# Optimization experiments

Hardware: AMD Instinct MI355X
Metric: run time of the kernel (lower is better)

## Reference

```python
import jax, jax.numpy as jnp
import numpy as np

N = 2_000_000
FEAT = 83      # mat_feature_len
DIMF = 64      # dim_features
LAT = 32       # latent_dim
INIT_RANGE = 0.02
SHIFT_INIT = 0.001
EPS = 1e-12


def setup_inputs() -> dict:
    key = jax.random.key(0)
    ks = jax.random.split(key, 8)
    inputs = jax.random.normal(ks[0], (N, FEAT), dtype=jnp.float32)
    keep = jax.random.bernoulli(ks[1], 0.5, (N,))
    inputs = inputs * keep[:, None].astype(jnp.float32)
    shift = jnp.full((1,), SHIFT_INIT, dtype=jnp.float32)  # ZeroShift scalar
    W1 = jax.random.normal(ks[2], (FEAT, DIMF), dtype=jnp.float32) * INIT_RANGE
    b1 = jnp.zeros((DIMF,), dtype=jnp.float32)
    Wh0 = jax.random.normal(ks[3], (DIMF, LAT), dtype=jnp.float32) * INIT_RANGE
    bh0 = jnp.zeros((LAT,), dtype=jnp.float32)
    Wh1 = jax.random.normal(ks[4], (LAT, LAT), dtype=jnp.float32) * INIT_RANGE
    bh1 = jnp.zeros((LAT,), dtype=jnp.float32)
    return {"inputs": inputs, "shift": shift, "W1": W1, "b1": b1,
            "Wh0": Wh0, "bh0": bh0, "Wh1": Wh1, "bh1": bh1}


def reference(inputs, shift, W1, b1, Wh0, bh0, Wh1, bh1):
    # mask_zero: a material row is valid iff any feature is nonzero
    mask = jnp.any(inputs != 0, axis=-1)  # (N,)
    # Original gathers valid rows, runs MLP, scatters back (zeros elsewhere).
    # All ops are row-wise, so compute densely and zero masked rows — same math.
    x = inputs + shift                            # ZeroShift (scalar shift)
    x = jax.nn.relu(x @ W1 + b1)                  # dens_1 -> (N, DIMF)
    x = jax.nn.relu(x @ Wh0 + bh0)                # hidden 0 -> (N, LAT)
    x = jax.nn.relu(x @ Wh1 + bh1)                # hidden 1 -> (N, LAT)
    # UnifyVector: L2-normalize rows
    norm = jnp.sqrt(jnp.sum(x * x, axis=-1, keepdims=True))
    emb = x / jnp.maximum(norm, EPS)
    emb = emb * mask[:, None].astype(emb.dtype)   # scatter_nd equivalent
    return (emb, emb, emb)
```

## Files before the change

kernel.cpp:

```cpp
#include <hip/hip_runtime.h>

#define FEAT 83
#define DIMF 64
#define LAT  32
#define THREADS 256
#define RPB  128

typedef __attribute__((ext_vector_type(8))) short bf16x8;
typedef __attribute__((ext_vector_type(4))) float f32x4;
typedef __attribute__((ext_vector_type(4))) unsigned u32x4;

#define WT1H 0
#define WT1L 6144
#define WT2H 12288
#define WT2L 14336
#define WT3H 16384
#define WT3L 17408
#define WS_SHORTS 18432

#define SM_SHORTS 26880

__device__ __forceinline__ short f2b(float f) {
    unsigned u = __float_as_uint(f);
    u += 0x7fffu + ((u >> 16) & 1u);
    return (short)(u >> 16);
}
__device__ __forceinline__ float b2f(short h) {
    return __uint_as_float(((unsigned)(unsigned short)h) << 16);
}

__global__ void prep_weights(const float* __restrict__ W1,
                             const float* __restrict__ Wh0,
                             const float* __restrict__ Wh1,
                             short* __restrict__ ws)
{
    const int stride = gridDim.x * blockDim.x;
    const int tid = blockIdx.x * blockDim.x + threadIdx.x;
    for (int idx = tid; idx < 64 * 96; idx += stride) {
        int c = idx / 96, k = idx - c * 96;
        float w = (k < FEAT) ? W1[k * 64 + c] : 0.f;
        short hi = f2b(w);
        ws[WT1H + idx] = hi;
        ws[WT1L + idx] = f2b(w - b2f(hi));
    }
    for (int idx = tid; idx < 32 * 64; idx += stride) {
        int c = idx >> 6, k = idx & 63;
        float w = Wh0[k * 32 + c];
        short hi = f2b(w);
        ws[WT2H + idx] = hi;
        ws[WT2L + idx] = f2b(w - b2f(hi));
    }
    for (int idx = tid; idx < 32 * 32; idx += stride) {
        int c = idx >> 5, k = idx & 31;
        float w = Wh1[k * 32 + c];
        short hi = f2b(w);
        ws[WT3H + idx] = hi;
        ws[WT3L + idx] = f2b(w - b2f(hi));
    }
}

__device__ __forceinline__ void unpack8(const unsigned* p, bf16x8& hi, bf16x8& lo) {
    union { bf16x8 v; unsigned u[4]; } H, L;
    #pragma unroll
    for (int d = 0; d < 4; ++d) {
        H.u[d] = __builtin_amdgcn_perm(p[2 * d + 1], p[2 * d], 0x07060302u);
        L.u[d] = __builtin_amdgcn_perm(p[2 * d + 1], p[2 * d], 0x05040100u);
    }
    hi = H.v; lo = L.v;
}

__global__ __launch_bounds__(THREADS, 3)
void material_encoder_kernel(const float* __restrict__ inp,
                             const float* __restrict__ shiftp,
                             const short* __restrict__ ws,
                             const float* __restrict__ b1,
                             const float* __restrict__ bh0,
                             const float* __restrict__ bh1,
                             float* __restrict__ out,
                             int nrows)
{
    __shared__ __align__(16) short sm[SM_SHORTS];
    unsigned* scr = (unsigned*)((char*)sm + 36864) + (threadIdx.x >> 6) * 1024;
    float* maskf  = (float*)((char*)sm + 53248);

    const int t    = threadIdx.x;
    const int lane = t & 63;
    const int wv   = t >> 6;
    const int lr   = lane & 15;
    const int lq   = (lane >> 4) & 3;

    float* xw = (float*)((char*)sm + wv * 10624);

    f32x4 xreg[11];
    {
        const f32x4* __restrict__ src4 = (const f32x4*)
            (inp + (long long)blockIdx.x * (RPB * FEAT) + wv * (32 * FEAT));
        #pragma unroll
        for (int r = 0; r < 10; ++r) xreg[r] = src4[r * 64 + lane];
        if (lane < 24) xreg[10] = src4[640 + lane];
    }
    f32x4 wreg[9];
    {
        const f32x4* __restrict__ wsrc = (const f32x4*)ws;
        #pragma unroll
        for (int it = 0; it < 9; ++it) wreg[it] = wsrc[it * THREADS + t];
    }
    {
        f32x4* xdst = (f32x4*)xw;
        #pragma unroll
        for (int r = 0; r < 10; ++r) xdst[r * 64 + lane] = xreg[r];
        if (lane < 24) xdst[640 + lane] = xreg[10];
    }

    float bias1[4], bias2[2], bias3[2];
    #pragma unroll
    for (int n = 0; n < 4; ++n) bias1[n] = b1[lr + 16 * n];
    #pragma unroll
    for (int n = 0; n < 2; ++n) { bias2[n] = bh0[lr + 16 * n]; bias3[n] = bh1[lr + 16 * n]; }
    const float sh = shiftp[0];
    const int Rw = blockIdx.x * RPB + wv * 32;

    bf16x8 a1h[2][3], a1l[2][3];
    float nzm[2];
    #pragma unroll
    for (int m = 0; m < 2; ++m) {
        const float* __restrict__ xr = xw + (16 * m + lr) * FEAT;
        float nz = 0.f;
        #pragma unroll
        for (int s = 0; s < 3; ++s) {
            const int k0 = 32 * s + 8 * lq;
            bf16x8 fh, fl;
            #pragma unroll
            for (int i = 0; i < 8; ++i) {
                int kk = k0 + i;
                kk = (kk < FEAT) ? kk : (FEAT - 1);
                const float x = xr[kk];
                nz = fmaxf(nz, fabsf(x));
                const float xs = x + sh;
                const unsigned u = __float_as_uint(xs);
                fh[i] = (short)(u >> 16);
                fl[i] = f2b(xs - __uint_as_float(u & 0xffff0000u));
            }
            a1h[m][s] = fh;
            a1l[m][s] = fl;
        }
        nzm[m] = nz;
    }
    #pragma unroll
    for (int m = 0; m < 2; ++m) {
        nzm[m] = fmaxf(nzm[m], __shfl_xor(nzm[m], 16));
        nzm[m] = fmaxf(nzm[m], __shfl_xor(nzm[m], 32));
    }
    if (lq == 0) {
        maskf[wv * 32 + lr]      = nzm[0];
        maskf[wv * 32 + 16 + lr] = nzm[1];
    }

    __syncthreads();

    {
        f32x4* wdst = (f32x4*)sm;
        #pragma unroll
        for (int it = 0; it < 9; ++it) wdst[it * THREADS + t] = wreg[it];
    }
    __syncthreads();

    f32x4 acc[2][4];
    #pragma unroll
    for (int m = 0; m < 2; ++m)
        #pragma unroll
        for (int n = 0; n < 4; ++n)
            acc[m][n] = (f32x4){bias1[n], bias1[n], bias1[n], bias1[n]};

    #pragma unroll
    for (int s = 0; s < 3; ++s)
        #pragma unroll
        for (int n = 0; n < 4; ++n) {
            bf16x8 bh = *(const bf16x8*)&sm[WT1H + (lr + 16 * n) * 96 + 32 * s + 8 * lq];
            bf16x8 bl = *(const bf16x8*)&sm[WT1L + (lr + 16 * n) * 96 + 32 * s + 8 * lq];
            #pragma unroll
            for (int m = 0; m < 2; ++m) {
                acc[m][n] = __builtin_amdgcn_mfma_f32_16x16x32_bf16(a1h[m][s], bh, acc[m][n], 0, 0, 0);
                acc[m][n] = __builtin_amdgcn_mfma_f32_16x16x32_bf16(a1l[m][s], bh, acc[m][n], 0, 0, 0);
                acc[m][n] = __builtin_amdgcn_mfma_f32_16x16x32_bf16(a1h[m][s], bl, acc[m][n], 0, 0, 0);
            }
        }

    f32x4 acc2[2][2];
    #pragma unroll
    for (int m = 0; m < 2; ++m)
        #pragma unroll
        for (int n = 0; n < 2; ++n)
            acc2[m][n] = (f32x4){bias2[n], bias2[n], bias2[n], bias2[n]};

    #pragma unroll
    for (int s = 0; s < 2; ++s) {
        #pragma unroll
        for (int m = 0; m < 2; ++m)
            #pragma unroll
            for (int np = 0; np < 2; ++np)
                #pragma unroll
                for (int r = 0; r < 4; ++r) {
                    const float hv = fmaxf(acc[m][2 * s + np][r], 0.f);
                    const unsigned u = __float_as_uint(hv);
                    const unsigned hiu = u & 0xffff0000u;
                    const unsigned lo16 =
                        (unsigned short)f2b(hv - __uint_as_float(hiu));
                    scr[(16 * m + 4 * lq + r) * 32 + lr + 16 * np] = hiu | lo16;
                }
        bf16x8 a2h[2], a2l[2];
        #pragma unroll
        for (int m = 0; m < 2; ++m) {
            unsigned p[8];
            *(u32x4*)&p[0] = *(const u32x4*)&scr[(lr + 16 * m) * 32 + 8 * lq];
            *(u32x4*)&p[4] = *(const u32x4*)&scr[(lr + 16 * m) * 32 + 8 * lq + 4];
            unpack8(p, a2h[m], a2l[m]);
        }
        #pragma unroll
        for (int n = 0; n < 2; ++n) {
            bf16x8 bh = *(const bf16x8*)&sm[WT2H + (lr + 16 * n) * 64 + 32 * s + 8 * lq];
            bf16x8 bl = *(const bf16x8*)&sm[WT2L + (lr + 16 * n) * 64 + 32 * s + 8 * lq];
            #pragma unroll
            for (int m = 0; m < 2; ++m) {
                acc2[m][n] = __builtin_amdgcn_mfma_f32_16x16x32_bf16(a2h[m], bh, acc2[m][n], 0, 0, 0);
                acc2[m][n] = __builtin_amdgcn_mfma_f32_16x16x32_bf16(a2l[m], bh, acc2[m][n], 0, 0, 0);
                acc2[m][n] = __builtin_amdgcn_mfma_f32_16x16x32_bf16(a2h[m], bl, acc2[m][n], 0, 0, 0);
            }
        }
    }

    f32x4 acc3[2][2];
    #pragma unroll
    for (int m = 0; m < 2; ++m)
        #pragma unroll
        for (int n = 0; n < 2; ++n)
            acc3[m][n] = (f32x4){bias3[n], bias3[n], bias3[n], bias3[n]};

    #pragma unroll
    for (int m = 0; m < 2; ++m)
        #pragma unroll
        for (int n = 0; n < 2; ++n)
            #pragma unroll
            for (int r = 0; r < 4; ++r) {
                const float gv = fmaxf(acc2[m][n][r], 0.f);
                const unsigned u = __float_as_uint(gv);
                const unsigned hiu = u & 0xffff0000u;
                const unsigned lo16 =
                    (unsigned short)f2b(gv - __uint_as_float(hiu));
                scr[(16 * m + 4 * lq + r) * 32 + lr + 16 * n] = hiu | lo16;
            }
    {
        bf16x8 a3h[2], a3l[2];
        #pragma unroll
        for (int m = 0; m < 2; ++m) {
            unsigned p[8];
            *(u32x4*)&p[0] = *(const u32x4*)&scr[(lr + 16 * m) * 32 + 8 * lq];
            *(u32x4*)&p[4] = *(const u32x4*)&scr[(lr + 16 * m) * 32 + 8 * lq + 4];
            unpack8(p, a3h[m], a3l[m]);
        }
        #pragma unroll
        for (int n = 0; n < 2; ++n) {
            bf16x8 bh = *(const bf16x8*)&sm[WT3H + (lr + 16 * n) * 32 + 8 * lq];
            bf16x8 bl = *(const bf16x8*)&sm[WT3L + (lr + 16 * n) * 32 + 8 * lq];
            #pragma unroll
            for (int m = 0; m < 2; ++m) {
                acc3[m][n] = __builtin_amdgcn_mfma_f32_16x16x32_bf16(a3h[m], bh, acc3[m][n], 0, 0, 0);
                acc3[m][n] = __builtin_amdgcn_mfma_f32_16x16x32_bf16(a3l[m], bh, acc3[m][n], 0, 0, 0);
                acc3[m][n] = __builtin_amdgcn_mfma_f32_16x16x32_bf16(a3h[m], bl, acc3[m][n], 0, 0, 0);
            }
        }
    }

    float er[2][2][4];
    float ssq[2][4];
    #pragma unroll
    for (int m = 0; m < 2; ++m)
        #pragma unroll
        for (int r = 0; r < 4; ++r) ssq[m][r] = 0.f;
    #pragma unroll
    for (int m = 0; m < 2; ++m)
        #pragma unroll
        for (int n = 0; n < 2; ++n)
            #pragma unroll
            for (int r = 0; r < 4; ++r) {
                float e = fmaxf(acc3[m][n][r], 0.f);
                er[m][n][r] = e;
                ssq[m][r] = fmaf(e, e, ssq[m][r]);
            }
    #pragma unroll
    for (int msk = 1; msk <= 8; msk <<= 1)
        #pragma unroll
        for (int m = 0; m < 2; ++m)
            #pragma unroll
            for (int r = 0; r < 4; ++r)
                ssq[m][r] += __shfl_xor(ssq[m][r], msk);

    const float* maskp = maskf + wv * 32;
    f32x4 mk[2];
    mk[0] = *(const f32x4*)&maskp[4 * lq];
    mk[1] = *(const f32x4*)&maskp[16 + 4 * lq];

    float sc[2][4];
    #pragma unroll
    for (int m = 0; m < 2; ++m)
        #pragma unroll
        for (int r = 0; r < 4; ++r)
            sc[m][r] = (mk[m][r] != 0.f) ? rsqrtf(fmaxf(ssq[m][r], 1e-24f)) : 0.f;

    const int osz = nrows * LAT;
    float* __restrict__ ob = out + (long long)Rw * LAT;
    #pragma unroll
    for (int m = 0; m < 2; ++m)
        #pragma unroll
        for (int r = 0; r < 4; ++r) {
            const int ro = (16 * m + 4 * lq + r) * LAT;
            #pragma unroll
            for (int n = 0; n < 2; ++n) {
                const float vv = er[m][n][r] * sc[m][r];
                const int cc = ro + lr + 16 * n;
                ob[cc]           = vv;
                ob[osz + cc]     = vv;
                ob[2 * osz + cc] = vv;
            }
        }
}

extern "C" void kernel_launch(void* const* d_in, const int* in_sizes, int n_in,
                              void* d_out, int out_size, void* d_ws, size_t ws_size,
                              hipStream_t stream) {
    const float* inp    = (const float*)d_in[0];
    const float* shiftp = (const float*)d_in[1];
    const float* W1     = (const float*)d_in[2];
    const float* b1     = (const float*)d_in[3];
    const float* Wh0    = (const float*)d_in[4];
    const float* bh0    = (const float*)d_in[5];
    const float* Wh1    = (const float*)d_in[6];
    const float* bh1    = (const float*)d_in[7];
    float* out = (float*)d_out;
    short* ws  = (short*)d_ws;

    const int nrows = in_sizes[0] / FEAT;
    const int blocks = nrows / RPB;

    prep_weights<<<dim3(24), dim3(THREADS), 0, stream>>>(W1, Wh0, Wh1, ws);
    material_encoder_kernel<<<dim3(blocks), dim3(THREADS), 0, stream>>>(
        inp, shiftp, ws, b1, bh0, bh1, out, nrows);
}
```

Before: 265.6 us.

## Read MFMA-fragment-packed weights directly from global memory, drop LDS weight staging

The weight prep kernel now writes the split bf16 weights in the exact per-lane MFMA fragment order, so the main kernel loads B operands straight from global (L2/L1-cached) with coalesced 16-byte loads instead of staging them into shared memory behind two block barriers. The row mask is now passed between lanes with shuffles instead of through LDS, and the block shrinks to 2 waves and 64 rows with about 21KB of LDS. This removes the barriers and the large LDS footprint, which should allow more resident blocks, at the cost of repeated global weight loads per wave that rely on cache hits.

```diff
diff --git a/kernel.cpp b/kernel.cpp
--- a/kernel.cpp
+++ b/kernel.cpp
@@ -3,22 +3,16 @@
 #define FEAT 83
 #define DIMF 64
 #define LAT  32
-#define THREADS 256
-#define RPB  128
+#define THREADS 128
+#define RPB  64
 
 typedef __attribute__((ext_vector_type(8))) short bf16x8;
 typedef __attribute__((ext_vector_type(4))) float f32x4;
 typedef __attribute__((ext_vector_type(4))) unsigned u32x4;
 
-#define WT1H 0
-#define WT1L 6144
-#define WT2H 12288
-#define WT2L 14336
-#define WT3H 16384
-#define WT3L 17408
 #define WS_SHORTS 18432
 
-#define SM_SHORTS 26880
+#define SM_BYTES (2 * 10624)
 
 __device__ __forceinline__ short f2b(float f) {
     unsigned u = __float_as_uint(f);
@@ -36,26 +30,37 @@
 {
     const int stride = gridDim.x * blockDim.x;
     const int tid = blockIdx.x * blockDim.x + threadIdx.x;
-    for (int idx = tid; idx < 64 * 96; idx += stride) {
-        int c = idx / 96, k = idx - c * 96;
-        float w = (k < FEAT) ? W1[k * 64 + c] : 0.f;
+    for (int idx = tid; idx < 12288; idx += stride) {
+        int p = idx >> 10, rem = idx & 1023;
+        int half = rem >> 9, e = rem & 511;
+        int l = e >> 3, i = e & 7;
+        int n = p / 3, s = p - 3 * n;
+        int c = (l & 15) + 16 * n;
+        int k = 32 * s + 8 * ((l >> 4) & 3) + i;
+        float w = (k < FEAT) ? W1[k * DIMF + c] : 0.f;
         short hi = f2b(w);
-        ws[WT1H + idx] = hi;
-        ws[WT1L + idx] = f2b(w - b2f(hi));
-    }
-    for (int idx = tid; idx < 32 * 64; idx += stride) {
-        int c = idx >> 6, k = idx & 63;
-        float w = Wh0[k * 32 + c];
+        ws[idx] = half ? f2b(w - b2f(hi)) : hi;
+    }
+    for (int idx = tid; idx < 4096; idx += stride) {
+        int p = idx >> 10, rem = idx & 1023;
+        int half = rem >> 9, e = rem & 511;
+        int l = e >> 3, i = e & 7;
+        int n = p >> 1, s = p & 1;
+        int c = (l & 15) + 16 * n;
+        int k = 32 * s + 8 * ((l >> 4) & 3) + i;
+        float w = Wh0[k * LAT + c];
         short hi = f2b(w);
-        ws[WT2H + idx] = hi;
-        ws[WT2L + idx] = f2b(w - b2f(hi));
-    }
-    for (int idx = tid; idx < 32 * 32; idx += stride) {
-        int c = idx >> 5, k = idx & 31;
-        float w = Wh1[k * 32 + c];
+        ws[12288 + idx] = half ? f2b(w - b2f(hi)) : hi;
+    }
+    for (int idx = tid; idx < 2048; idx += stride) {
+        int n = idx >> 10, rem = idx & 1023;
+        int half = rem >> 9, e = rem & 511;
+        int l = e >> 3, i = e & 7;
+        int c = (l & 15) + 16 * n;
+        int k = 8 * ((l >> 4) & 3) + i;
+        float w = Wh1[k * LAT + c];
         short hi = f2b(w);
-        ws[WT3H + idx] = hi;
-        ws[WT3L + idx] = f2b(w - b2f(hi));
+        ws[16384 + idx] = half ? f2b(w - b2f(hi)) : hi;
     }
 }
 
@@ -79,9 +84,7 @@
                              float* __restrict__ out,
                              int nrows)
 {
-    __shared__ __align__(16) short sm[SM_SHORTS];
-    unsigned* scr = (unsigned*)((char*)sm + 36864) + (threadIdx.x >> 6) * 1024;
-    float* maskf  = (float*)((char*)sm + 53248);
+    __shared__ __align__(16) char smb[SM_BYTES];
 
     const int t    = threadIdx.x;
     const int lane = t & 63;
@@ -89,7 +92,8 @@
     const int lr   = lane & 15;
     const int lq   = (lane >> 4) & 3;
 
-    float* xw = (float*)((char*)sm + wv * 10624);
+    float*    xw  = (float*)(smb + wv * 10624);
+    unsigned* scr = (unsigned*)(smb + wv * 10624);
 
     f32x4 xreg[11];
     {
@@ -98,12 +102,6 @@
         #pragma unroll
         for (int r = 0; r < 10; ++r) xreg[r] = src4[r * 64 + lane];
         if (lane < 24) xreg[10] = src4[640 + lane];
-    }
-    f32x4 wreg[9];
-    {
-        const f32x4* __restrict__ wsrc = (const f32x4*)ws;
-        #pragma unroll
-        for (int it = 0; it < 9; ++it) wreg[it] = wsrc[it * THREADS + t];
     }
     {
         f32x4* xdst = (f32x4*)xw;
@@ -151,19 +149,8 @@
         nzm[m] = fmaxf(nzm[m], __shfl_xor(nzm[m], 16));
         nzm[m] = fmaxf(nzm[m], __shfl_xor(nzm[m], 32));
     }
-    if (lq == 0) {
-        maskf[wv * 32 + lr]      = nzm[0];
-        maskf[wv * 32 + 16 + lr] = nzm[1];
-    }
-
-    __syncthreads();
-
-    {
-        f32x4* wdst = (f32x4*)sm;
-        #pragma unroll
-        for (int it = 0; it < 9; ++it) wdst[it * THREADS + t] = wreg[it];
-    }
-    __syncthreads();
+
+    const bf16x8* __restrict__ wf = (const bf16x8*)ws;
 
     f32x4 acc[2][4];
     #pragma unroll
@@ -176,8 +163,9 @@
     for (int s = 0; s < 3; ++s)
         #pragma unroll
         for (int n = 0; n < 4; ++n) {
-            bf16x8 bh = *(const bf16x8*)&sm[WT1H + (lr + 16 * n) * 96 + 32 * s + 8 * lq];
-            bf16x8 bl = *(const bf16x8*)&sm[WT1L + (lr + 16 * n) * 96 + 32 * s + 8 * lq];
+            const int p = (n * 3 + s) * 128;
+            bf16x8 bh = wf[p + lane];
+            bf16x8 bl = wf[p + 64 + lane];
             #pragma unroll
             for (int m = 0; m < 2; ++m) {
                 acc[m][n] = __builtin_amdgcn_mfma_f32_16x16x32_bf16(a1h[m][s], bh, acc[m][n], 0, 0, 0);
@@ -218,8 +206,9 @@
         }
         #pragma unroll
         for (int n = 0; n < 2; ++n) {
-            bf16x8 bh = *(const bf16x8*)&sm[WT2H + (lr + 16 * n) * 64 + 32 * s + 8 * lq];
-            bf16x8 bl = *(const bf16x8*)&sm[WT2L + (lr + 16 * n) * 64 + 32 * s + 8 * lq];
+            const int p = 1536 + (n * 2 + s) * 128;
+            bf16x8 bh = wf[p + lane];
+            bf16x8 bl = wf[p + 64 + lane];
             #pragma unroll
             for (int m = 0; m < 2; ++m) {
                 acc2[m][n] = __builtin_amdgcn_mfma_f32_16x16x32_bf16(a2h[m], bh, acc2[m][n], 0, 0, 0);
@@ -260,8 +249,9 @@
         }
         #pragma unroll
         for (int n = 0; n < 2; ++n) {
-            bf16x8 bh = *(const bf16x8*)&sm[WT3H + (lr + 16 * n) * 32 + 8 * lq];
-            bf16x8 bl = *(const bf16x8*)&sm[WT3L + (lr + 16 * n) * 32 + 8 * lq];
+            const int p = 2048 + n * 128;
+            bf16x8 bh = wf[p + lane];
+            bf16x8 bl = wf[p + 64 + lane];
             #pragma unroll
             for (int m = 0; m < 2; ++m) {
                 acc3[m][n] = __builtin_amdgcn_mfma_f32_16x16x32_bf16(a3h[m], bh, acc3[m][n], 0, 0, 0);
@@ -295,17 +285,14 @@
             for (int r = 0; r < 4; ++r)
                 ssq[m][r] += __shfl_xor(ssq[m][r], msk);
 
-    const float* maskp = maskf + wv * 32;
-    f32x4 mk[2];
-    mk[0] = *(const f32x4*)&maskp[4 * lq];
-    mk[1] = *(const f32x4*)&maskp[16 + 4 * lq];
-
     float sc[2][4];
     #pragma unroll
     for (int m = 0; m < 2; ++m)
         #pragma unroll
-        for (int r = 0; r < 4; ++r)
-            sc[m][r] = (mk[m][r] != 0.f) ? rsqrtf(fmaxf(ssq[m][r], 1e-24f)) : 0.f;
+        for (int r = 0; r < 4; ++r) {
+            const float mkv = __shfl(nzm[m], 4 * lq + r);
+            sc[m][r] = (mkv != 0.f) ? rsqrtf(fmaxf(ssq[m][r], 1e-24f)) : 0.f;
+        }
 
     const int osz = nrows * LAT;
     float* __restrict__ ob = out + (long long)Rw * LAT;
@@ -342,7 +329,7 @@
     const int nrows = in_sizes[0] / FEAT;
     const int blocks = nrows / RPB;
 
-    prep_weights<<<dim3(24), dim3(THREADS), 0, stream>>>(W1, Wh0, Wh1, ws);
+    prep_weights<<<dim3(24), dim3(256), 0, stream>>>(W1, Wh0, Wh1, ws);
     material_encoder_kernel<<<dim3(blocks), dim3(THREADS), 0, stream>>>(
         inp, shiftp, ws, b1, bh0, bh1, out, nrows);
 }
```

After: 306.9 us. +15.6%, slower.

## Convert to persistent grid-stride kernel with register prefetch of next tile

Applied to the files above, without the earlier changes.

Replaces one-block-per-128-rows launch with a persistent grid of 512 blocks of 128 threads, each looping over 64-row tiles with the next tile's input prefetched into registers while the MFMA chain runs. Weights are loaded into shared memory once per block instead of once per tile, and the input staging area is double-buffered per wave. The mask is now kept in registers via shuffles instead of shared memory. The risk is lower occupancy (launch bounds 1, 512 small blocks on 256 CUs) which may reduce memory-level parallelism for this bandwidth-bound kernel.

```diff
diff --git a/kernel.cpp b/kernel.cpp
--- a/kernel.cpp
+++ b/kernel.cpp
@@ -3,8 +3,9 @@
 #define FEAT 83
 #define DIMF 64
 #define LAT  32
-#define THREADS 256
-#define RPB  128
+#define THREADS 128
+#define TROWS 64
+#define GRID 512
 
 typedef __attribute__((ext_vector_type(8))) short bf16x8;
 typedef __attribute__((ext_vector_type(4))) float f32x4;
@@ -18,7 +19,7 @@
 #define WT3L 17408
 #define WS_SHORTS 18432
 
-#define SM_SHORTS 26880
+#define SM_BYTES (36864 + 2 * 21248)
 
 __device__ __forceinline__ short f2b(float f) {
     unsigned u = __float_as_uint(f);
@@ -69,7 +70,7 @@
     hi = H.v; lo = L.v;
 }
 
-__global__ __launch_bounds__(THREADS, 3)
+__global__ __launch_bounds__(THREADS, 1)
 void material_encoder_kernel(const float* __restrict__ inp,
                              const float* __restrict__ shiftp,
                              const short* __restrict__ ws,
@@ -79,9 +80,8 @@
                              float* __restrict__ out,
                              int nrows)
 {
-    __shared__ __align__(16) short sm[SM_SHORTS];
-    unsigned* scr = (unsigned*)((char*)sm + 36864) + (threadIdx.x >> 6) * 1024;
-    float* maskf  = (float*)((char*)sm + 53248);
+    __shared__ __align__(16) char smb[SM_BYTES];
+    short* sm = (short*)smb;
 
     const int t    = threadIdx.x;
     const int lane = t & 63;
@@ -89,27 +89,12 @@
     const int lr   = lane & 15;
     const int lq   = (lane >> 4) & 3;
 
-    float* xw = (float*)((char*)sm + wv * 10624);
-
-    f32x4 xreg[11];
-    {
-        const f32x4* __restrict__ src4 = (const f32x4*)
-            (inp + (long long)blockIdx.x * (RPB * FEAT) + wv * (32 * FEAT));
-        #pragma unroll
-        for (int r = 0; r < 10; ++r) xreg[r] = src4[r * 64 + lane];
-        if (lane < 24) xreg[10] = src4[640 + lane];
-    }
-    f32x4 wreg[9];
     {
         const f32x4* __restrict__ wsrc = (const f32x4*)ws;
-        #pragma unroll
-        for (int it = 0; it < 9; ++it) wreg[it] = wsrc[it * THREADS + t];
-    }
-    {
-        f32x4* xdst = (f32x4*)xw;
-        #pragma unroll
-        for (int r = 0; r < 10; ++r) xdst[r * 64 + lane] = xreg[r];
-        if (lane < 24) xdst[640 + lane] = xreg[10];
+        f32x4* wdst = (f32x4*)smb;
+        #pragma unroll
+        for (int it = 0; it < 18; ++it)
+            wdst[it * THREADS + t] = wsrc[it * THREADS + t];
     }
 
     float bias1[4], bias2[2], bias3[2];
@@ -118,211 +103,237 @@
     #pragma unroll
     for (int n = 0; n < 2; ++n) { bias2[n] = bh0[lr + 16 * n]; bias3[n] = bh1[lr + 16 * n]; }
     const float sh = shiftp[0];
-    const int Rw = blockIdx.x * RPB + wv * 32;
-
-    bf16x8 a1h[2][3], a1l[2][3];
-    float nzm[2];
-    #pragma unroll
-    for (int m = 0; m < 2; ++m) {
-        const float* __restrict__ xr = xw + (16 * m + lr) * FEAT;
-        float nz = 0.f;
-        #pragma unroll
-        for (int s = 0; s < 3; ++s) {
-            const int k0 = 32 * s + 8 * lq;
-            bf16x8 fh, fl;
-            #pragma unroll
-            for (int i = 0; i < 8; ++i) {
-                int kk = k0 + i;
-                kk = (kk < FEAT) ? kk : (FEAT - 1);
-                const float x = xr[kk];
-                nz = fmaxf(nz, fabsf(x));
-                const float xs = x + sh;
-                const unsigned u = __float_as_uint(xs);
-                fh[i] = (short)(u >> 16);
-                fl[i] = f2b(xs - __uint_as_float(u & 0xffff0000u));
-            }
-            a1h[m][s] = fh;
-            a1l[m][s] = fl;
-        }
-        nzm[m] = nz;
-    }
-    #pragma unroll
-    for (int m = 0; m < 2; ++m) {
-        nzm[m] = fmaxf(nzm[m], __shfl_xor(nzm[m], 16));
-        nzm[m] = fmaxf(nzm[m], __shfl_xor(nzm[m], 32));
-    }
-    if (lq == 0) {
-        maskf[wv * 32 + lr]      = nzm[0];
-        maskf[wv * 32 + 16 + lr] = nzm[1];
-    }
 
     __syncthreads();
 
+    const int ntiles = nrows / TROWS;
+    const int osz    = nrows * LAT;
+    char* xchunk0 = smb + 36864 + wv * 21248;
+
+    int tile = blockIdx.x;
+    f32x4 xreg[11];
     {
-        f32x4* wdst = (f32x4*)sm;
-        #pragma unroll
-        for (int it = 0; it < 9; ++it) wdst[it * THREADS + t] = wreg[it];
-    }
-    __syncthreads();
-
-    f32x4 acc[2][4];
-    #pragma unroll
-    for (int m = 0; m < 2; ++m)
-        #pragma unroll
-        for (int n = 0; n < 4; ++n)
-            acc[m][n] = (f32x4){bias1[n], bias1[n], bias1[n], bias1[n]};
-
-    #pragma unroll
-    for (int s = 0; s < 3; ++s)
-        #pragma unroll
-        for (int n = 0; n < 4; ++n) {
-            bf16x8 bh = *(const bf16x8*)&sm[WT1H + (lr + 16 * n) * 96 + 32 * s + 8 * lq];
-            bf16x8 bl = *(const bf16x8*)&sm[WT1L + (lr + 16 * n) * 96 + 32 * s + 8 * lq];
+        const f32x4* __restrict__ src4 = (const f32x4*)
+            (inp + (long long)tile * (TROWS * FEAT) + wv * (32 * FEAT));
+        #pragma unroll
+        for (int r = 0; r < 10; ++r) xreg[r] = src4[r * 64 + lane];
+        if (lane < 24) xreg[10] = src4[640 + lane];
+    }
+
+    int parity = 0;
+    for (;;) {
+        float*    xw  = (float*)(xchunk0 + parity * 10624);
+        unsigned* scr = (unsigned*)xw;
+
+        {
+            f32x4* xdst = (f32x4*)xw;
+            #pragma unroll
+            for (int r = 0; r < 10; ++r) xdst[r * 64 + lane] = xreg[r];
+            if (lane < 24) xdst[640 + lane] = xreg[10];
+        }
+
+        bf16x8 a1h[2][3], a1l[2][3];
+        float nzm[2];
+        #pragma unroll
+        for (int m = 0; m < 2; ++m) {
+            const float* __restrict__ xr = xw + (16 * m + lr) * FEAT;
+            float nz = 0.f;
+            #pragma unroll
+            for (int s = 0; s < 3; ++s) {
+                const int k0 = 32 * s + 8 * lq;
+                bf16x8 fh, fl;
+                #pragma unroll
+                for (int i = 0; i < 8; ++i) {
+                    int kk = k0 + i;
+                    kk = (kk < FEAT) ? kk : (FEAT - 1);
+                    const float x = xr[kk];
+                    nz = fmaxf(nz, fabsf(x));
+                    const float xs = x + sh;
+                    const unsigned u = __float_as_uint(xs);
+                    fh[i] = (short)(u >> 16);
+                    fl[i] = f2b(xs - __uint_as_float(u & 0xffff0000u));
+                }
+                a1h[m][s] = fh;
+                a1l[m][s] = fl;
+            }
+            nzm[m] = nz;
+        }
+        #pragma unroll
+        for (int m = 0; m < 2; ++m) {
+            nzm[m] = fmaxf(nzm[m], __shfl_xor(nzm[m], 16));
+            nzm[m] = fmaxf(nzm[m], __shfl_xor(nzm[m], 32));
+        }
+
+        const int next = tile + GRID;
+        const bool has_next = next < ntiles;
+        if (has_next) {
+            const f32x4* __restrict__ src4 = (const f32x4*)
+                (inp + (long long)next * (TROWS * FEAT) + wv * (32 * FEAT));
+            #pragma unroll
+            for (int r = 0; r < 10; ++r) xreg[r] = src4[r * 64 + lane];
+            if (lane < 24) xreg[10] = src4[640 + lane];
+        }
+
+        f32x4 acc[2][4];
+        #pragma unroll
+        for (int m = 0; m < 2; ++m)
+            #pragma unroll
+            for (int n = 0; n < 4; ++n)
+                acc[m][n] = (f32x4){bias1[n], bias1[n], bias1[n], bias1[n]};
+
+        #pragma unroll
+        for (int s = 0; s < 3; ++s)
+            #pragma unroll
+            for (int n = 0; n < 4; ++n) {
+                bf16x8 bh = *(const bf16x8*)&sm[WT1H + (lr + 16 * n) * 96 + 32 * s + 8 * lq];
+                bf16x8 bl = *(const bf16x8*)&sm[WT1L + (lr + 16 * n) * 96 + 32 * s + 8 * lq];
+                #pragma unroll
+                for (int m = 0; m < 2; ++m) {
+                    acc[m][n] = __builtin_amdgcn_mfma_f32_16x16x32_bf16(a1h[m][s], bh, acc[m][n], 0, 0, 0);
+                    acc[m][n] = __builtin_amdgcn_mfma_f32_16x16x32_bf16(a1l[m][s], bh, acc[m][n], 0, 0, 0);
+                    acc[m][n] = __builtin_amdgcn_mfma_f32_16x16x32_bf16(a1h[m][s], bl, acc[m][n], 0, 0, 0);
+                }
+            }
+
+        f32x4 acc2[2][2];
+        #pragma unroll
+        for (int m = 0; m < 2; ++m)
+            #pragma unroll
+            for (int n = 0; n < 2; ++n)
+                acc2[m][n] = (f32x4){bias2[n], bias2[n], bias2[n], bias2[n]};
+
+        #pragma unroll
+        for (int s = 0; s < 2; ++s) {
+            #pragma unroll
+            for (int m = 0; m < 2; ++m)
+                #pragma unroll
+                for (int np = 0; np < 2; ++np)
+                    #pragma unroll
+                    for (int r = 0; r < 4; ++r) {
+                        const float hv = fmaxf(acc[m][2 * s + np][r], 0.f);
+                        const unsigned u = __float_as_uint(hv);
+                        const unsigned hiu = u & 0xffff0000u;
+                        const unsigned lo16 =
+                            (unsigned short)f2b(hv - __uint_as_float(hiu));
+                        scr[(16 * m + 4 * lq + r) * 32 + lr + 16 * np] = hiu | lo16;
+                    }
+            bf16x8 a2h[2], a2l[2];
             #pragma unroll
             for (int m = 0; m < 2; ++m) {
-                acc[m][n] = __builtin_amdgcn_mfma_f32_16x16x32_bf16(a1h[m][s], bh, acc[m][n], 0, 0, 0);
-                acc[m][n] = __builtin_amdgcn_mfma_f32_16x16x32_bf16(a1l[m][s], bh, acc[m][n], 0, 0, 0);
-                acc[m][n] = __builtin_amdgcn_mfma_f32_16x16x32_bf16(a1h[m][s], bl, acc[m][n], 0, 0, 0);
-            }
-        }
-
-    f32x4 acc2[2][2];
-    #pragma unroll
-    for (int m = 0; m < 2; ++m)
-        #pragma unroll
-        for (int n = 0; n < 2; ++n)
-            acc2[m][n] = (f32x4){bias2[n], bias2[n], bias2[n], bias2[n]};
-
-    #pragma unroll
-    for (int s = 0; s < 2; ++s) {
-        #pragma unroll
-        for (int m = 0; m < 2; ++m)
-            #pragma unroll
-            for (int np = 0; np < 2; ++np)
+                unsigned p[8];
+                *(u32x4*)&p[0] = *(const u32x4*)&scr[(lr + 16 * m) * 32 + 8 * lq];
+                *(u32x4*)&p[4] = *(const u32x4*)&scr[(lr + 16 * m) * 32 + 8 * lq + 4];
+                unpack8(p, a2h[m], a2l[m]);
+            }
+            #pragma unroll
+            for (int n = 0; n < 2; ++n) {
+                bf16x8 bh = *(const bf16x8*)&sm[WT2H + (lr + 16 * n) * 64 + 32 * s + 8 * lq];
+                bf16x8 bl = *(const bf16x8*)&sm[WT2L + (lr + 16 * n) * 64 + 32 * s + 8 * lq];
+                #pragma unroll
+                for (int m = 0; m < 2; ++m) {
+                    acc2[m][n] = __builtin_amdgcn_mfma_f32_16x16x32_bf16(a2h[m], bh, acc2[m][n], 0, 0, 0);
+                    acc2[m][n] = __builtin_amdgcn_mfma_f32_16x16x32_bf16(a2l[m], bh, acc2[m][n], 0, 0, 0);
+                    acc2[m][n] = __builtin_amdgcn_mfma_f32_16x16x32_bf16(a2h[m], bl, acc2[m][n], 0, 0, 0);
+                }
+            }
+        }
+
+        f32x4 acc3[2][2];
+        #pragma unroll
+        for (int m = 0; m < 2; ++m)
+            #pragma unroll
+            for (int n = 0; n < 2; ++n)
+                acc3[m][n] = (f32x4){bias3[n], bias3[n], bias3[n], bias3[n]};
+
+        #pragma unroll
+        for (int m = 0; m < 2; ++m)
+            #pragma unroll
+            for (int n = 0; n < 2; ++n)
                 #pragma unroll
                 for (int r = 0; r < 4; ++r) {
-                    const float hv = fmaxf(acc[m][2 * s + np][r], 0.f);
-                    const unsigned u = __float_as_uint(hv);
+                    const float gv = fmaxf(acc2[m][n][r], 0.f);
+                    const unsigned u = __float_as_uint(gv);
                     const unsigned hiu = u & 0xffff0000u;
                     const unsigned lo16 =
-                        (unsigned short)f2b(hv - __uint_as_float(hiu));
-                    scr[(16 * m + 4 * lq + r) * 32 + lr + 16 * np] = hiu | lo16;
-                }
-        bf16x8 a2h[2], a2l[2];
-        #pragma unroll
-        for (int m = 0; m < 2; ++m) {
-            unsigned p[8];
-            *(u32x4*)&p[0] = *(const u32x4*)&scr[(lr + 16 * m) * 32 + 8 * lq];
-            *(u32x4*)&p[4] = *(const u32x4*)&scr[(lr + 16 * m) * 32 + 8 * lq + 4];
-            unpack8(p, a2h[m], a2l[m]);
-        }
-        #pragma unroll
-        for (int n = 0; n < 2; ++n) {
-            bf16x8 bh = *(const bf16x8*)&sm[WT2H + (lr + 16 * n) * 64 + 32 * s + 8 * lq];
-            bf16x8 bl = *(const bf16x8*)&sm[WT2L + (lr + 16 * n) * 64 + 32 * s + 8 * lq];
+                        (unsigned short)f2b(gv - __uint_as_float(hiu));
+                    scr[(16 * m + 4 * lq + r) * 32 + lr + 16 * n] = hiu | lo16;
+                }
+        {
+            bf16x8 a3h[2], a3l[2];
             #pragma unroll
             for (int m = 0; m < 2; ++m) {
-                acc2[m][n] = __builtin_amdgcn_mfma_f32_16x16x32_bf16(a2h[m], bh, acc2[m][n], 0, 0, 0);
-                acc2[m][n] = __builtin_amdgcn_mfma_f32_16x16x32_bf16(a2l[m], bh, acc2[m][n], 0, 0, 0);
-                acc2[m][n] = __builtin_amdgcn_mfma_f32_16x16x32_bf16(a2h[m], bl, acc2[m][n], 0, 0, 0);
-            }
-        }
-    }
-
-    f32x4 acc3[2][2];
-    #pragma unroll
-    for (int m = 0; m < 2; ++m)
-        #pragma unroll
-        for (int n = 0; n < 2; ++n)
-            acc3[m][n] = (f32x4){bias3[n], bias3[n], bias3[n], bias3[n]};
-
-    #pragma unroll
-    for (int m = 0; m < 2; ++m)
-        #pragma unroll
-        for (int n = 0; n < 2; ++n)
+                unsigned p[8];
+                *(u32x4*)&p[0] = *(const u32x4*)&scr[(lr + 16 * m) * 32 + 8 * lq];
+                *(u32x4*)&p[4] = *(const u32x4*)&scr[(lr + 16 * m) * 32 + 8 * lq + 4];
+                unpack8(p, a3h[m], a3l[m]);
+            }
+            #pragma unroll
+            for (int n = 0; n < 2; ++n) {
+                bf16x8 bh = *(const bf16x8*)&sm[WT3H + (lr + 16 * n) * 32 + 8 * lq];
+                bf16x8 bl = *(const bf16x8*)&sm[WT3L + (lr + 16 * n) * 32 + 8 * lq];
+                #pragma unroll
+                for (int m = 0; m < 2; ++m) {
+                    acc3[m][n] = __builtin_amdgcn_mfma_f32_16x16x32_bf16(a3h[m], bh, acc3[m][n], 0, 0, 0);
+                    acc3[m][n] = __builtin_amdgcn_mfma_f32_16x16x32_bf16(a3l[m], bh, acc3[m][n], 0, 0, 0);
+                    acc3[m][n] = __builtin_amdgcn_mfma_f32_16x16x32_bf16(a3h[m], bl, acc3[m][n], 0, 0, 0);
+                }
+            }
+        }
+
+        float er[2][2][4];
+        float ssq[2][4];
+        #pragma unroll
+        for (int m = 0; m < 2; ++m)
+            #pragma unroll
+            for (int r = 0; r < 4; ++r) ssq[m][r] = 0.f;
+        #pragma unroll
+        for (int m = 0; m < 2; ++m)
+            #pragma unroll
+            for (int n = 0; n < 2; ++n)
+                #pragma unroll
+                for (int r = 0; r < 4; ++r) {
+                    float e = fmaxf(acc3[m][n][r], 0.f);
+                    er[m][n][r] = e;
+                    ssq[m][r] = fmaf(e, e, ssq[m][r]);
+                }
+        #pragma unroll
+        for (int msk = 1; msk <= 8; msk <<= 1)
+            #pragma unroll
+            for (int m = 0; m < 2; ++m)
+                #pragma unroll
+                for (int r = 0; r < 4; ++r)
+                    ssq[m][r] += __shfl_xor(ssq[m][r], msk);
+
+        float sc[2][4];
+        #pragma unroll
+        for (int m = 0; m < 2; ++m)
             #pragma unroll
             for (int r = 0; r < 4; ++r) {
-                const float gv = fmaxf(acc2[m][n][r], 0.f);
-                const unsigned u = __float_as_uint(gv);
-                const unsigned hiu = u & 0xffff0000u;
-                const unsigned lo16 =
-                    (unsigned short)f2b(gv - __uint_as_float(hiu));
-                scr[(16 * m + 4 * lq + r) * 32 + lr + 16 * n] = hiu | lo16;
-            }
-    {
-        bf16x8 a3h[2], a3l[2];
-        #pragma unroll
-        for (int m = 0; m < 2; ++m) {
-            unsigned p[8];
-            *(u32x4*)&p[0] = *(const u32x4*)&scr[(lr + 16 * m) * 32 + 8 * lq];
-            *(u32x4*)&p[4] = *(const u32x4*)&scr[(lr + 16 * m) * 32 + 8 * lq + 4];
-            unpack8(p, a3h[m], a3l[m]);
-        }
-        #pragma unroll
-        for (int n = 0; n < 2; ++n) {
-            bf16x8 bh = *(const bf16x8*)&sm[WT3H + (lr + 16 * n) * 32 + 8 * lq];
-            bf16x8 bl = *(const bf16x8*)&sm[WT3L + (lr + 16 * n) * 32 + 8 * lq];
-            #pragma unroll
-            for (int m = 0; m < 2; ++m) {
-                acc3[m][n] = __builtin_amdgcn_mfma_f32_16x16x32_bf16(a3h[m], bh, acc3[m][n], 0, 0, 0);
-                acc3[m][n] = __builtin_amdgcn_mfma_f32_16x16x32_bf16(a3l[m], bh, acc3[m][n], 0, 0, 0);
-                acc3[m][n] = __builtin_amdgcn_mfma_f32_16x16x32_bf16(a3h[m], bl, acc3[m][n], 0, 0, 0);
-            }
-        }
-    }
-
-    float er[2][2][4];
-    float ssq[2][4];
-    #pragma unroll
-    for (int m = 0; m < 2; ++m)
-        #pragma unroll
-        for (int r = 0; r < 4; ++r) ssq[m][r] = 0.f;
-    #pragma unroll
-    for (int m = 0; m < 2; ++m)
-        #pragma unroll
-        for (int n = 0; n < 2; ++n)
+                const float mkv = __shfl(nzm[m], 4 * lq + r);
+                sc[m][r] = (mkv != 0.f) ? rsqrtf(fmaxf(ssq[m][r], 1e-24f)) : 0.f;
+            }
+
+        const int Rw = tile * TROWS + wv * 32;
+        float* __restrict__ ob = out + (long long)Rw * LAT;
+        #pragma unroll
+        for (int m = 0; m < 2; ++m)
             #pragma unroll
             for (int r = 0; r < 4; ++r) {
-                float e = fmaxf(acc3[m][n][r], 0.f);
-                er[m][n][r] = e;
-                ssq[m][r] = fmaf(e, e, ssq[m][r]);
-            }
-    #pragma unroll
-    for (int msk = 1; msk <= 8; msk <<= 1)
-        #pragma unroll
-        for (int m = 0; m < 2; ++m)
-            #pragma unroll
-            for (int r = 0; r < 4; ++r)
-                ssq[m][r] += __shfl_xor(ssq[m][r], msk);
-
-    const float* maskp = maskf + wv * 32;
-    f32x4 mk[2];
-    mk[0] = *(const f32x4*)&maskp[4 * lq];
-    mk[1] = *(const f32x4*)&maskp[16 + 4 * lq];
-
-    float sc[2][4];
-    #pragma unroll
-    for (int m = 0; m < 2; ++m)
-        #pragma unroll
-        for (int r = 0; r < 4; ++r)
-            sc[m][r] = (mk[m][r] != 0.f) ? rsqrtf(fmaxf(ssq[m][r], 1e-24f)) : 0.f;
-
-    const int osz = nrows * LAT;
-    float* __restrict__ ob = out + (long long)Rw * LAT;
-    #pragma unroll
-    for (int m = 0; m < 2; ++m)
-        #pragma unroll
-        for (int r = 0; r < 4; ++r) {
-            const int ro = (16 * m + 4 * lq + r) * LAT;
-            #pragma unroll
-            for (int n = 0; n < 2; ++n) {
-                const float vv = er[m][n][r] * sc[m][r];
-                const int cc = ro + lr + 16 * n;
-                ob[cc]           = vv;
-                ob[osz + cc]     = vv;
-                ob[2 * osz + cc] = vv;
-            }
-        }
+                const int ro = (16 * m + 4 * lq + r) * LAT;
+                #pragma unroll
+                for (int n = 0; n < 2; ++n) {
+                    const float vv = er[m][n][r] * sc[m][r];
+                    const int cc = ro + lr + 16 * n;
+                    ob[cc]           = vv;
+                    ob[osz + cc]     = vv;
+                    ob[2 * osz + cc] = vv;
+                }
+            }
+
+        if (!has_next) break;
+        tile = next;
+        parity ^= 1;
+    }
 }
 
 extern "C" void kernel_launch(void* const* d_in, const int* in_sizes, int n_in,
@@ -339,10 +350,11 @@
     float* out = (float*)d_out;
     short* ws  = (short*)d_ws;
 
-    const int nrows = in_sizes[0] / FEAT;
-    const int blocks = nrows / RPB;
-
-    prep_weights<<<dim3(24), dim3(THREADS), 0, stream>>>(W1, Wh0, Wh1, ws);
-    material_encoder_kernel<<<dim3(blocks), dim3(THREADS), 0, stream>>>(
+    const int nrows  = in_sizes[0] / FEAT;
+    const int ntiles = nrows / TROWS;
+    const int grid   = (ntiles < GRID) ? ntiles : GRID;
+
+    prep_weights<<<dim3(24), dim3(256), 0, stream>>>(W1, Wh0, Wh1, ws);
+    material_encoder_kernel<<<dim3(grid), dim3(THREADS), 0, stream>>>(
         inp, shiftp, ws, b1, bh0, bh1, out, nrows);
 }
```

Result: slower. 285.9 us (+7.6%).
